# Performance work log

Hardware: AMD Instinct MI355X
Metric: run time of the kernel (lower is better)

Reference implementation:

```python
import jax, jax.numpy as jnp
import numpy as np

D = 2048          # input_size
B_NECK = 512      # bottleneck_size
NUM_LANGS = 16
ZETA = 1.1
GAMMA = -0.1
LN_EPS = 1e-5


def setup_inputs() -> dict:
    key = jax.random.key(0)
    ks = jax.random.split(key, 8)
    x = jax.random.normal(ks[0], (8, 2048, D), dtype=jnp.float32)
    # xavier_uniform for linear weights
    lim_d = float(np.sqrt(6.0 / (D + B_NECK)))
    down_w = jax.random.uniform(ks[1], (B_NECK, D), minval=-lim_d, maxval=lim_d, dtype=jnp.float32)
    up_w = jax.random.uniform(ks[2], (D, B_NECK), minval=-lim_d, maxval=lim_d, dtype=jnp.float32)
    down_b = jnp.zeros((B_NECK,), dtype=jnp.float32)
    up_b = jnp.zeros((D,), dtype=jnp.float32)
    ln_g = jnp.ones((D,), dtype=jnp.float32)
    ln_b = jnp.zeros((D,), dtype=jnp.float32)
    down_loga = 0.01 * jax.random.normal(ks[3], (NUM_LANGS, D), dtype=jnp.float32)
    up_loga = 0.01 * jax.random.normal(ks[4], (NUM_LANGS, B_NECK), dtype=jnp.float32)
    return {"x": x, "down_w": down_w, "down_b": down_b, "up_w": up_w,
            "up_b": up_b, "ln_g": ln_g, "ln_b": ln_b,
            "down_loga": down_loga, "up_loga": up_loga, "lang_id": 3}


def _det_mask(loga_row):
    # eval-mode L0 gate: hardtanh(sigmoid(loga)*(zeta-gamma)+gamma, 0, 1)
    return jnp.clip(jax.nn.sigmoid(loga_row) * (ZETA - GAMMA) + GAMMA, 0.0, 1.0)


def reference(x, down_w, down_b, up_w, up_b, ln_g, ln_b, down_loga, up_loga, lang_id):
    shortcut = x
    # LayerNorm over last dim
    mu = jnp.mean(x, axis=-1, keepdims=True)
    var = jnp.mean(jnp.square(x - mu), axis=-1, keepdims=True)
    h = (x - mu) * jax.lax.rsqrt(var + LN_EPS) * ln_g + ln_b
    # down projection with per-input-feature gate (mask scales weight columns)
    dmask = _det_mask(down_loga[lang_id])            # [D]
    h = jnp.einsum('bsd,kd->bsk', h * dmask, down_w) + down_b  # [B,S,B_NECK]
    h = jax.nn.relu(h)
    # up projection with per-bottleneck gate
    umask = _det_mask(up_loga[lang_id])              # [B_NECK]
    h = jnp.einsum('bsk,dk->bsd', h * umask, up_w) + up_b       # [B,S,D]
    return h + shortcut
```

## Files before the change

### kernel.cpp

```cpp
#include <hip/hip_runtime.h>
#include <cstdint>
#include <cstddef>

typedef unsigned short u16;
typedef __attribute__((ext_vector_type(4))) float f32x4;
typedef __attribute__((ext_vector_type(8))) short bf16x8;

#define LN_EPS 1e-5f

__device__ __forceinline__ u16 f2bf(float f) {
  unsigned int u = __float_as_uint(f);
  u += 0x7FFFu + ((u >> 16) & 1u);
  return (u16)(u >> 16);
}

__device__ __forceinline__ float l0gate(float loga) {
  float s = 1.0f / (1.0f + expf(-loga));
  float v = s * 1.2f - 0.1f;
  return fminf(fmaxf(v, 0.0f), 1.0f);
}

__device__ __forceinline__ void llds16(u16* lds, const u16* g) {
  __builtin_amdgcn_global_load_lds(
      (const __attribute__((address_space(1))) unsigned int*)g,
      (__attribute__((address_space(3))) unsigned int*)lds, 16, 0, 0);
}

__global__ __launch_bounds__(256) void prep_weights(
    const float* __restrict__ dw, const float* __restrict__ uw,
    const float* __restrict__ dloga, const float* __restrict__ uloga,
    const int* __restrict__ lang,
    u16* __restrict__ dwb, u16* __restrict__ uwb) {
  const int lid = lang[0];
  const unsigned i = blockIdx.x * 256u + threadIdx.x;
  dwb[i] = f2bf(dw[i] * l0gate(dloga[lid * 2048 + (i & 2047u)]));
  uwb[i] = f2bf(uw[i] * l0gate(uloga[lid * 512 + (i & 511u)]));
}

__global__ __launch_bounds__(256) void ln_kernel(
    const float* __restrict__ x, const float* __restrict__ g,
    const float* __restrict__ b, u16* __restrict__ h1) {
  const int row = blockIdx.x;
  const int tid = threadIdx.x;
  const float4* xr = (const float4*)(x + (size_t)row * 2048);
  float4 v0 = xr[tid * 2 + 0];
  float4 v1 = xr[tid * 2 + 1];
  float s = v0.x + v0.y + v0.z + v0.w + v1.x + v1.y + v1.z + v1.w;
  float q = v0.x * v0.x + v0.y * v0.y + v0.z * v0.z + v0.w * v0.w +
            v1.x * v1.x + v1.y * v1.y + v1.z * v1.z + v1.w * v1.w;
#pragma unroll
  for (int off = 32; off > 0; off >>= 1) {
    s += __shfl_down(s, off, 64);
    q += __shfl_down(q, off, 64);
  }
  __shared__ float ss[4], sq[4], sstat[2];
  const int wave = tid >> 6, lane = tid & 63;
  if (lane == 0) { ss[wave] = s; sq[wave] = q; }
  __syncthreads();
  if (tid == 0) {
    float S = ss[0] + ss[1] + ss[2] + ss[3];
    float Q = sq[0] + sq[1] + sq[2] + sq[3];
    float mu = S * (1.0f / 2048.0f);
    float var = Q * (1.0f / 2048.0f) - mu * mu;
    sstat[0] = mu;
    sstat[1] = rsqrtf(var + LN_EPS);
  }
  __syncthreads();
  const float mu = sstat[0], rs = sstat[1];
  const float4* g4 = (const float4*)g;
  const float4* b4 = (const float4*)b;
  float4 ga = g4[tid * 2], gb = g4[tid * 2 + 1];
  float4 ba = b4[tid * 2], bb = b4[tid * 2 + 1];
  union { u16 us[8]; uint4 u; } p;
  p.us[0] = f2bf((v0.x - mu) * rs * ga.x + ba.x);
  p.us[1] = f2bf((v0.y - mu) * rs * ga.y + ba.y);
  p.us[2] = f2bf((v0.z - mu) * rs * ga.z + ba.z);
  p.us[3] = f2bf((v0.w - mu) * rs * ga.w + ba.w);
  p.us[4] = f2bf((v1.x - mu) * rs * gb.x + bb.x);
  p.us[5] = f2bf((v1.y - mu) * rs * gb.y + bb.y);
  p.us[6] = f2bf((v1.z - mu) * rs * gb.z + bb.z);
  p.us[7] = f2bf((v1.w - mu) * rs * gb.w + bb.w);
  ((uint4*)(h1 + (size_t)row * 2048))[tid] = p.u;
}

template <int EPI>
__global__ __launch_bounds__(256) void gemm_bt(
    const u16* __restrict__ A, const u16* __restrict__ B,
    int M, int N, int K,
    const float* __restrict__ bias,
    const float* __restrict__ resid,
    void* __restrict__ outp) {
  __shared__ u16 As[2][128 * 64];
  __shared__ u16 Bs[2][128 * 64];
  const int tid = threadIdx.x;
  const int wave = tid >> 6, lane = tid & 63;
  const int wr = (wave >> 1) * 64;
  const int wc = (wave & 1) * 64;
  const int lrow = lane & 15, lk = lane >> 4;
  const size_t m0 = (size_t)blockIdx.y * 128;
  const size_t n0 = (size_t)blockIdx.x * 128;
  const int srow = lane >> 3;
  const int scol = (lane & 7) * 8;

  f32x4 acc[4][4] = {};

  auto STAGE = [&](int buf, int k0) {
#pragma unroll
    for (int c = 0; c < 4; ++c) {
      const int seg = c * 4 + wave;
      const int r = seg * 8 + srow;
      llds16(&As[buf][seg * 512], A + (m0 + r) * (size_t)K + (k0 + scol));
      llds16(&Bs[buf][seg * 512], B + (n0 + r) * (size_t)K + (k0 + scol));
    }
  };

  STAGE(0, 0);
  __syncthreads();

  int cur = 0;
  for (int k0 = 0; k0 < K; k0 += 64) {
    if (k0 + 64 < K) STAGE(cur ^ 1, k0 + 64);

    const u16* Ab = &As[cur][0];
    const u16* Bb = &Bs[cur][0];
#pragma unroll
    for (int ks = 0; ks < 2; ++ks) {
      bf16x8 af[4], bfr[4];
#pragma unroll
      for (int m = 0; m < 4; ++m)
        af[m] = *(const bf16x8*)&Ab[(wr + m * 16 + lrow) * 64 + ks * 32 + lk * 8];
#pragma unroll
      for (int n = 0; n < 4; ++n)
        bfr[n] = *(const bf16x8*)&Bb[(wc + n * 16 + lrow) * 64 + ks * 32 + lk * 8];
      __builtin_amdgcn_s_setprio(1);
#pragma unroll
      for (int m = 0; m < 4; ++m)
#pragma unroll
        for (int n = 0; n < 4; ++n)
          acc[m][n] = __builtin_amdgcn_mfma_f32_16x16x32_bf16(af[m], bfr[n],
                                                              acc[m][n], 0, 0, 0);
      __builtin_amdgcn_s_setprio(0);
    }
    __syncthreads();
    cur ^= 1;
  }

#pragma unroll
  for (int m = 0; m < 4; ++m) {
    const size_t row_base = m0 + wr + m * 16 + lk * 4;
#pragma unroll
    for (int n = 0; n < 4; ++n) {
      const size_t col = n0 + wc + n * 16 + lrow;
      const float bv = bias[col];
#pragma unroll
      for (int r = 0; r < 4; ++r) {
        const size_t row = row_base + r;
        float v = acc[m][n][r] + bv;
        if (EPI == 1) {
          v = fmaxf(v, 0.0f);
          ((u16*)outp)[row * (size_t)N + col] = f2bf(v);
        } else {
          v += resid[row * (size_t)N + col];
          ((float*)outp)[row * (size_t)N + col] = v;
        }
      }
    }
  }
}

extern "C" void kernel_launch(void* const* d_in, const int* in_sizes, int n_in,
                              void* d_out, int out_size, void* d_ws, size_t ws_size,
                              hipStream_t stream) {
  const float* x         = (const float*)d_in[0];
  const float* down_w    = (const float*)d_in[1];
  const float* down_b    = (const float*)d_in[2];
  const float* up_w      = (const float*)d_in[3];
  const float* up_b      = (const float*)d_in[4];
  const float* ln_g      = (const float*)d_in[5];
  const float* ln_b      = (const float*)d_in[6];
  const float* down_loga = (const float*)d_in[7];
  const float* up_loga   = (const float*)d_in[8];
  const int*   lang      = (const int*)d_in[9];

  const int D = 2048, BNK = 512;
  const int M = in_sizes[0] / D;

  char* ws = (char*)d_ws;
  u16* h1  = (u16*)ws;
  u16* h2  = (u16*)(ws + (size_t)M * D * 2);
  u16* dwb = (u16*)(ws + (size_t)M * D * 2 + (size_t)M * BNK * 2);
  u16* uwb = dwb + (size_t)BNK * D;

  prep_weights<<<(BNK * D) / 256, 256, 0, stream>>>(down_w, up_w, down_loga,
                                                    up_loga, lang, dwb, uwb);
  ln_kernel<<<M, 256, 0, stream>>>(x, ln_g, ln_b, h1);
  gemm_bt<1><<<dim3(BNK / 128, M / 128), 256, 0, stream>>>(
      h1, dwb, M, BNK, D, down_b, nullptr, h2);
  gemm_bt<2><<<dim3(D / 128, M / 128), 256, 0, stream>>>(
      h2, uwb, M, D, BNK, up_b, x, d_out);
}
```

Before: 178.7 us.

## Swizzle GEMM LDS layout, remap workgroups across XCDs, refine pipeline waits

The GEMM now stages A and B into LDS with an XOR swizzle on the 16-byte column slot and reads fragments through the same swizzle, to cut LDS bank conflicts on the MFMA operand loads. The launch becomes a 1-D grid whose block index is permuted so that consecutive tiles land on the same XCD, aiming at better L2 reuse of shared A and B panels. The double-buffer loop replaces __syncthreads with explicit vmcnt/lgkmcnt waits and raw barriers, so the next tile's prefetch stays in flight while the current one is consumed. The remap assumes the workgroup count is divisible by 8, and the hand-written waitcnt values depend on the exact number of loads issued per stage.

```diff
diff --git a/kernel.cpp b/kernel.cpp
--- a/kernel.cpp
+++ b/kernel.cpp
@@ -86,7 +86,7 @@
 template <int EPI>
 __global__ __launch_bounds__(256) void gemm_bt(
     const u16* __restrict__ A, const u16* __restrict__ B,
-    int M, int N, int K,
+    int M, int N, int K, int NX,
     const float* __restrict__ bias,
     const float* __restrict__ resid,
     void* __restrict__ outp) {
@@ -97,29 +97,40 @@
   const int wr = (wave >> 1) * 64;
   const int wc = (wave & 1) * 64;
   const int lrow = lane & 15, lk = lane >> 4;
-  const size_t m0 = (size_t)blockIdx.y * 128;
-  const size_t n0 = (size_t)blockIdx.x * 128;
+
+  const int nwg = gridDim.x;
+  const int wg = (blockIdx.x & 7) * (nwg >> 3) + (blockIdx.x >> 3);
+  const int bx = wg % NX, by = wg / NX;
+  const size_t m0 = (size_t)by * 128;
+  const size_t n0 = (size_t)bx * 128;
+
+  f32x4 acc[4][4] = {};
+
   const int srow = lane >> 3;
-  const int scol = (lane & 7) * 8;
-
-  f32x4 acc[4][4] = {};
-
+  const int sslot = (lane & 7) ^ ((lane >> 3) & 7);
   auto STAGE = [&](int buf, int k0) {
 #pragma unroll
     for (int c = 0; c < 4; ++c) {
       const int seg = c * 4 + wave;
       const int r = seg * 8 + srow;
-      llds16(&As[buf][seg * 512], A + (m0 + r) * (size_t)K + (k0 + scol));
-      llds16(&Bs[buf][seg * 512], B + (n0 + r) * (size_t)K + (k0 + scol));
+      llds16(&As[buf][seg * 512], A + (m0 + r) * (size_t)K + (k0 + sslot * 8));
+      llds16(&Bs[buf][seg * 512], B + (n0 + r) * (size_t)K + (k0 + sslot * 8));
     }
   };
 
+  const int NT = K >> 6;
   STAGE(0, 0);
-  __syncthreads();
-
-  int cur = 0;
-  for (int k0 = 0; k0 < K; k0 += 64) {
-    if (k0 + 64 < K) STAGE(cur ^ 1, k0 + 64);
+
+  for (int t = 0; t < NT; ++t) {
+    const int cur = t & 1;
+    if (t + 1 < NT) {
+      STAGE(cur ^ 1, (t + 1) << 6);
+      asm volatile("s_waitcnt vmcnt(8)" ::: "memory");
+    } else {
+      asm volatile("s_waitcnt vmcnt(0)" ::: "memory");
+    }
+    __builtin_amdgcn_s_barrier();
+    asm volatile("" ::: "memory");
 
     const u16* Ab = &As[cur][0];
     const u16* Bb = &Bs[cur][0];
@@ -128,10 +139,12 @@
       bf16x8 af[4], bfr[4];
 #pragma unroll
       for (int m = 0; m < 4; ++m)
-        af[m] = *(const bf16x8*)&Ab[(wr + m * 16 + lrow) * 64 + ks * 32 + lk * 8];
+        af[m] = *(const bf16x8*)&Ab[(wr + m * 16 + lrow) * 64 +
+                                    ((unsigned)(ks * 4 + lk) ^ (lane & 7)) * 8];
 #pragma unroll
       for (int n = 0; n < 4; ++n)
-        bfr[n] = *(const bf16x8*)&Bb[(wc + n * 16 + lrow) * 64 + ks * 32 + lk * 8];
+        bfr[n] = *(const bf16x8*)&Bb[(wc + n * 16 + lrow) * 64 +
+                                     ((unsigned)(ks * 4 + lk) ^ (lane & 7)) * 8];
       __builtin_amdgcn_s_setprio(1);
 #pragma unroll
       for (int m = 0; m < 4; ++m)
@@ -141,8 +154,9 @@
                                                               acc[m][n], 0, 0, 0);
       __builtin_amdgcn_s_setprio(0);
     }
-    __syncthreads();
-    cur ^= 1;
+    asm volatile("s_waitcnt lgkmcnt(0)" ::: "memory");
+    __builtin_amdgcn_s_barrier();
+    asm volatile("" ::: "memory");
   }
 
 #pragma unroll
@@ -194,8 +208,10 @@
   prep_weights<<<(BNK * D) / 256, 256, 0, stream>>>(down_w, up_w, down_loga,
                                                     up_loga, lang, dwb, uwb);
   ln_kernel<<<M, 256, 0, stream>>>(x, ln_g, ln_b, h1);
-  gemm_bt<1><<<dim3(BNK / 128, M / 128), 256, 0, stream>>>(
-      h1, dwb, M, BNK, D, down_b, nullptr, h2);
-  gemm_bt<2><<<dim3(D / 128, M / 128), 256, 0, stream>>>(
-      h2, uwb, M, D, BNK, up_b, x, d_out);
-}
+  const int nwg1 = (BNK / 128) * (M / 128);
+  const int nwg2 = (D / 128) * (M / 128);
+  gemm_bt<1><<<nwg1, 256, 0, stream>>>(h1, dwb, M, BNK, D, BNK / 128,
+                                       down_b, nullptr, h2);
+  gemm_bt<2><<<nwg2, 256, 0, stream>>>(h2, uwb, M, D, BNK, D / 128,
+                                       up_b, x, d_out);
+}
```

After: 159.3 us. -10.9%, faster.
